# Kernel optimization log

Hardware: AMD Instinct MI355X
Metric: run time of the kernel (lower is better)

The kernel has to match this reference:

```python
import jax, jax.numpy as jnp
import numpy as np

B, Q, D, H, EF = 64, 300, 512, 8, 4
DH = D // H            # 64, per-head dim for scores
DV = (D * EF) // H     # 256, per-head value dim


def setup_inputs() -> dict:
    key = jax.random.key(0)
    ks = jax.random.split(key, 10)
    s = 0.02
    return {
        "query_feats": jax.random.normal(ks[0], (B, Q, D), jnp.float32),
        "bias": jax.random.normal(ks[1], (1, H, Q, Q), jnp.float32),
        "W_gen": jax.random.normal(ks[2], (D, D), jnp.float32) * s,
        "b_gen": jax.random.normal(ks[3], (D,), jnp.float32) * s,
        "W_val": jax.random.normal(ks[4], (D, D * EF), jnp.float32) * s,
        "b_val": jax.random.normal(ks[5], (D * EF,), jnp.float32) * s,
        "W_out": jax.random.normal(ks[6], (D * EF, D), jnp.float32) * s,
        "b_out": jax.random.normal(ks[7], (D,), jnp.float32) * s,
        "weight_bank": jnp.ones((1, H, Q, Q), jnp.float32) / np.sqrt(DH).astype(np.float32),
    }


def reference(query_feats, bias, W_gen, b_gen, W_val, b_val, W_out, b_out, weight_bank):
    bs, nq, d = query_feats.shape
    h = weight_bank.shape[1]
    # params_generator -> dynamic mixing matrix M: [bs, h, dh, nq]
    M = (query_feats @ W_gen + b_gen).reshape(bs, nq, h, -1).transpose(0, 2, 3, 1)
    # value: [bs, h, nq, dv]
    value = (query_feats @ W_val + b_val).reshape(bs, nq, h, -1).transpose(0, 2, 1, 3)
    # queries split per head: [bs, h, nq, dh]
    q = query_feats.reshape(bs, nq, h, -1).transpose(0, 2, 1, 3)
    # scores: [bs, h, nq, nq], scaled by learned weight bank + bias, GELU (exact), softmax
    scores = jnp.einsum('bhqd,bhdk->bhqk', q, M) * weight_bank + bias
    attn = jax.nn.softmax(jax.nn.gelu(scores, approximate=False), axis=-1)
    out = jnp.einsum('bhqk,bhkv->bhqv', attn, value)
    out = out.transpose(0, 2, 1, 3).reshape(bs, nq, -1)
    out = out @ W_out + b_out
    return out + query_feats
```

## Files before the change

### kernel.cpp

```cpp
#include <hip/hip_runtime.h>
#include <hip/hip_bf16.h>

typedef __attribute__((ext_vector_type(4))) float f32x4;
typedef __attribute__((ext_vector_type(8))) short s16x8;
typedef __attribute__((ext_vector_type(4))) short s16x4;
typedef __attribute__((ext_vector_type(4))) unsigned int u32x4;

#define MFMA16(A, B, C) __builtin_amdgcn_mfma_f32_16x16x32_bf16((A), (B), (C), 0, 0, 0)

#define GLDS16(gsrc, ldst) __builtin_amdgcn_global_load_lds(                   \
    (const __attribute__((address_space(1))) void*)(gsrc),                    \
    (__attribute__((address_space(3))) void*)(ldst), 16, 0, 0)

__device__ __forceinline__ ushort f2bf(float f) {
    __hip_bfloat16 h = __float2bfloat16(f);
    return *reinterpret_cast<ushort*>(&h);
}

__device__ __forceinline__ float exp_gelu(float x) {
    float u = x * x;
    float m = fmaf(-0.1029439065f, u, -2.3022154392f);
    float e2 = __builtin_amdgcn_exp2f(x * m);
    float g = x * __builtin_amdgcn_rcpf(1.0f + e2);
    return __expf(g);
}

__global__ __launch_bounds__(256) void k_prep(const float* __restrict__ qf,
                                              ushort* __restrict__ qf_bf,
                                              const float* __restrict__ W_gen,
                                              const float* __restrict__ W_val,
                                              const float* __restrict__ W_out,
                                              const float* __restrict__ wb,
                                              const float* __restrict__ bias,
                                              ushort* __restrict__ WgvT,
                                              ushort* __restrict__ WoT,
                                              unsigned int* __restrict__ wbbT,
                                              ushort* __restrict__ Vt) {
    __shared__ float tile[32][33];
    __shared__ float tb[32][33];
    int blk = blockIdx.x;
    int tx = threadIdx.x & 31, ty = threadIdx.x >> 5;
    if (blk < 9600) {
        int i = (blk * 256 + threadIdx.x) * 4;
        float4 v = *(const float4*)(qf + i);
        ushort4 o;
        o.x = f2bf(v.x); o.y = f2bf(v.y); o.z = f2bf(v.z); o.w = f2bf(v.w);
        *(ushort4*)(qf_bf + i) = o;
        return;
    }
    blk -= 9600;
    if (blk < 2304) {
        const float* w; ushort* wt; int K, N, kx, ny;
        if (blk < 256)       { w = W_gen; wt = WgvT;             K = 512;  N = 512;
                               kx = blk & 15;          ny = blk >> 4; }
        else if (blk < 1280) { w = W_val; wt = WgvT + 512 * 512; K = 512;  N = 2048;
                               int b2 = blk - 256;  kx = b2 & 15; ny = b2 >> 4; }
        else                 { w = W_out; wt = WoT;              K = 2048; N = 512;
                               int b2 = blk - 1280; kx = b2 & 63; ny = b2 >> 6; }
        int k0 = kx * 32, n0 = ny * 32;
        #pragma unroll
        for (int i = ty; i < 32; i += 8)
            tile[i][tx] = w[(size_t)(k0 + i) * N + n0 + tx];
        __syncthreads();
        #pragma unroll
        for (int i = ty; i < 32; i += 8)
            wt[(size_t)(n0 + i) * K + k0 + tx] = f2bf(tile[tx][i]);
        return;
    }
    blk -= 2304;
    if (blk < 800) {
        int h = blk / 100, rem = blk - h * 100;
        int kx = rem / 10, qx = rem - kx * 10;
        int k0 = kx * 32, q0 = qx * 32;
        #pragma unroll
        for (int i = ty; i < 32; i += 8)
            if (q0 + i < 300 && k0 + tx < 300) {
                size_t si = ((size_t)h * 300 + q0 + i) * 300 + k0 + tx;
                tile[i][tx] = wb[si];
                tb[i][tx]   = bias[si];
            }
        __syncthreads();
        #pragma unroll
        for (int i = ty; i < 32; i += 8)
            if (k0 + i < 300 && q0 + tx < 300) {
                int k = k0 + i;
                unsigned int pk = (unsigned int)f2bf(tile[tx][i])
                                | ((unsigned int)f2bf(tb[tx][i]) << 16);
                wbbT[(((size_t)h * 75 + (k >> 2)) * 300 + (q0 + tx)) * 4 + (k & 3)] = pk;
            }
        return;
    }
    blk -= 800;
    int tid = blk * 256 + threadIdx.x;
    int bh = tid >> 8, v = tid & 255;
    *(s16x4*)(Vt + (size_t)bh * 77824 + 73728 + v * 16 + 12) = (s16x4){0, 0, 0, 0};
}

template <int OUT>
__global__ __launch_bounds__(512, 2) void k_gemm256(const ushort* __restrict__ A,
                                                    const ushort* __restrict__ BT,
                                                    const float* __restrict__ b1,
                                                    const float* __restrict__ b2,
                                                    void* __restrict__ o1,
                                                    void* __restrict__ o2,
                                                    int K, int GY) {
    __shared__ __align__(16) ushort As[2][256 * 64];
    __shared__ __align__(16) ushort Bs[2][256 * 64];
    int id = blockIdx.x;
    int xcd = id & 7, s = id >> 3;
    int mxl = s / GY, ny = s - mxl * GY;
    int mx = xcd * 10 + mxl;
    if (mx >= 75) return;
    int m0 = mx * 256, n0g = ny * 256;

    int t = threadIdx.x, l = t & 63, w = t >> 6;
    int wr = w >> 2, wc = w & 3;
    int lr = l & 15, lg = l >> 4;

    int rsrc[4], ksrc[4];
    #pragma unroll
    for (int c8 = 0; c8 < 4; ++c8) {
        int o = (c8 * 512 + t) * 16;
        int op = o ^ (((o >> 7) & 7) << 4);
        rsrc[c8] = op >> 7;
        ksrc[c8] = (op & 127) >> 1;
    }

    auto stage = [&](int kt, int buf) {
        int k0 = kt * 64;
        ushort* AsB = &As[buf][0];
        ushort* BsB = &Bs[buf][0];
        #pragma unroll
        for (int c8 = 0; c8 < 4; ++c8) {
            int dst = (c8 * 512 + w * 64) * 8;
            GLDS16(A  + (size_t)(m0 + rsrc[c8]) * K + k0 + ksrc[c8], AsB + dst);
            GLDS16(BT + (size_t)(n0g + rsrc[c8]) * K + k0 + ksrc[c8], BsB + dst);
        }
    };

    f32x4 acc[8][4];
    #pragma unroll
    for (int i = 0; i < 8; ++i)
        #pragma unroll
        for (int j = 0; j < 4; ++j)
            acc[i][j] = (f32x4){0.f, 0.f, 0.f, 0.f};

    int NT = K >> 6;
    stage(0, 0);
    stage(1, 1);

    for (int kt = 0; kt < NT; ++kt) {
        if (kt + 1 < NT) asm volatile("s_waitcnt vmcnt(8)" ::: "memory");
        else             asm volatile("s_waitcnt vmcnt(0)" ::: "memory");
        __builtin_amdgcn_s_barrier();

        int cur = kt & 1;
        const char* Ab = (const char*)&As[cur][0];
        const char* Bb = (const char*)&Bs[cur][0];
        #pragma unroll
        for (int ks = 0; ks < 2; ++ks) {
            int kb = (ks * 64 + lg * 16) ^ ((lr & 7) << 4);
            s16x8 af[8], bfv[4];
            #pragma unroll
            for (int rt = 0; rt < 8; ++rt)
                af[rt] = *(const s16x8*)(Ab + (wr * 128 + rt * 16 + lr) * 128 + kb);
            #pragma unroll
            for (int ct = 0; ct < 4; ++ct)
                bfv[ct] = *(const s16x8*)(Bb + (wc * 64 + ct * 16 + lr) * 128 + kb);
            #pragma unroll
            for (int rt = 0; rt < 8; ++rt)
                #pragma unroll
                for (int ct = 0; ct < 4; ++ct)
                    acc[rt][ct] = MFMA16(af[rt], bfv[ct], acc[rt][ct]);
        }

        __builtin_amdgcn_s_barrier();
        if (kt + 2 < NT) stage(kt + 2, cur);
    }

    if (OUT == 0) {
        if (n0g < 512) {
            ushort* G = (ushort*)o1;
            #pragma unroll
            for (int rt = 0; rt < 8; ++rt)
                #pragma unroll
                for (int ct = 0; ct < 4; ++ct) {
                    int col = n0g + wc * 64 + ct * 16 + lr;
                    float bv = b1[col];
                    #pragma unroll
                    for (int rr = 0; rr < 4; ++rr) {
                        int row = m0 + wr * 128 + rt * 16 + lg * 4 + rr;
                        G[(size_t)row * 512 + col] = f2bf(acc[rt][ct][rr] + bv);
                    }
                }
        } else {
            ushort* Vt = (ushort*)o2;
            #pragma unroll
            for (int rt = 0; rt < 8; ++rt) {
                int rl0 = m0 + wr * 128 + rt * 16 + lg * 4;
                int bb = rl0 / 300, key0 = rl0 - bb * 300;
                #pragma unroll
                for (int ct = 0; ct < 4; ++ct) {
                    int colv = n0g - 512 + wc * 64 + ct * 16 + lr;
                    float bv = b2[colv];
                    int hh = colv >> 8, v = colv & 255;
                    s16x4 pw;
                    #pragma unroll
                    for (int rr = 0; rr < 4; ++rr)
                        pw[rr] = (short)f2bf(acc[rt][ct][rr] + bv);
                    size_t bhb = (size_t)(bb * 8 + hh) * 77824;
                    size_t addr = (key0 < 288)
                        ? bhb + (size_t)(key0 >> 5) * 8192 + v * 32 + (key0 & 31)
                        : bhb + 73728 + v * 16 + (key0 - 288);
                    *(s16x4*)(Vt + addr) = pw;
                }
            }
        }
    } else {
        float* out = (float*)o1;
        #pragma unroll
        for (int rt = 0; rt < 8; ++rt)
            #pragma unroll
            for (int ct = 0; ct < 4; ++ct) {
                int col = n0g + wc * 64 + ct * 16 + lr;
                float bv = b1[col];
                #pragma unroll
                for (int rr = 0; rr < 4; ++rr) {
                    int row = m0 + wr * 128 + rt * 16 + lg * 4 + rr;
                    size_t idx = (size_t)row * 512 + col;
                    out[idx] = acc[rt][ct][rr] + bv + b2[idx];
                }
            }
    }
}

__global__ __launch_bounds__(512, 6) void k_attn(const ushort* __restrict__ qf_bf,
                                                 const ushort* __restrict__ G_bf,
                                                 const ushort* __restrict__ Vt,
                                                 const unsigned int* __restrict__ wbb,
                                                 ushort* __restrict__ O) {
    __shared__ __align__(16) ushort P[64 * 320];
    __shared__ float partial[2][64];
    int id = blockIdx.x;
    int xcd = id & 7, s = id >> 3;
    int h = s / 40; int r2 = s - h * 40;
    int bi = r2 / 5, qt = r2 - bi * 5;
    int b = xcd * 8 + bi;

    int t = threadIdx.x, l = t & 63, w = t >> 6;
    int lr = l & 15, lg = l >> 4;
    int wq = w & 3, wk = w >> 2;

    auto p_addr = [&](int q, int k) -> ushort* {
        int byte = (q * 640 + k * 2) ^ ((q & 15) << 4);
        return (ushort*)((char*)P + byte);
    };

    int qr = min(qt * 64 + wq * 16 + lr, 299);
    const ushort* qp = qf_bf + ((size_t)(b * 300 + qr)) * 512 + h * 64 + lg * 8;
    s16x8 q0 = *(const s16x8*)(qp);
    s16x8 q1 = *(const s16x8*)(qp + 32);

    const unsigned int* wbbq = wbb + (size_t)h * 90000 + qr * 4;

    int qq = wq * 16 + lr;
    float ssum = 0.f;
    int ktlo = wk * 10, kthi = min(ktlo + 10, 18);
    const unsigned int* wp = wbbq + (size_t)(ktlo * 4 + lg) * 1200;
    const ushort* gp = G_bf + ((size_t)(b * 300) + ktlo * 16 + lr) * 512 + h * 64 + lg * 8;

    s16x8 g0 = *(const s16x8*)(gp);
    s16x8 g1 = *(const s16x8*)(gp + 32);
    u32x4 uv = *(const u32x4*)(wp);

    for (int kt = ktlo; kt < kthi - 1; ++kt) {
        const ushort* gpn = gp + 16 * 512;
        const unsigned int* wpn = wp + 4800;
        s16x8 ng0 = *(const s16x8*)(gpn);
        s16x8 ng1 = *(const s16x8*)(gpn + 32);
        u32x4 nuv = *(const u32x4*)(wpn);

        f32x4 a = (f32x4){0.f, 0.f, 0.f, 0.f};
        a = MFMA16(g0, q0, a);
        a = MFMA16(g1, q1, a);
        int kbase = kt * 16 + lg * 4;
        s16x4 pw;
        #pragma unroll
        for (int r = 0; r < 4; ++r) {
            unsigned int u = uv[r];
            float wv = __builtin_bit_cast(float, u << 16);
            float bv = __builtin_bit_cast(float, u & 0xffff0000u);
            float x = fmaf(a[r], wv, bv);
            float p = exp_gelu(x);
            ssum += p;
            pw[r] = (short)f2bf(p);
        }
        *(s16x4*)p_addr(qq, kbase) = pw;
        g0 = ng0; g1 = ng1; uv = nuv; gp = gpn; wp = wpn;
    }
    {
        f32x4 a = (f32x4){0.f, 0.f, 0.f, 0.f};
        a = MFMA16(g0, q0, a);
        a = MFMA16(g1, q1, a);
        int kbase = (kthi - 1) * 16 + lg * 4;
        s16x4 pw;
        #pragma unroll
        for (int r = 0; r < 4; ++r) {
            unsigned int u = uv[r];
            float wv = __builtin_bit_cast(float, u << 16);
            float bv = __builtin_bit_cast(float, u & 0xffff0000u);
            float x = fmaf(a[r], wv, bv);
            float p = exp_gelu(x);
            ssum += p;
            pw[r] = (short)f2bf(p);
        }
        *(s16x4*)p_addr(qq, kbase) = pw;
    }
    if (wk == 1) {
        int kcl = min(288 + lr, 299);
        const ushort* gpe = G_bf + ((size_t)(b * 300 + kcl)) * 512 + h * 64 + lg * 8;
        s16x8 e0 = *(const s16x8*)(gpe);
        s16x8 e1 = *(const s16x8*)(gpe + 32);
        f32x4 a = (f32x4){0.f, 0.f, 0.f, 0.f};
        a = MFMA16(e0, q0, a);
        a = MFMA16(e1, q1, a);
        int kbase = 288 + lg * 4;
        int g4 = min(72 + lg, 74);
        u32x4 ev = *(const u32x4*)(wbbq + (size_t)g4 * 1200);
        s16x4 pw;
        #pragma unroll
        for (int r = 0; r < 4; ++r) {
            unsigned int u = ev[r];
            float wv = __builtin_bit_cast(float, u << 16);
            float bv = __builtin_bit_cast(float, u & 0xffff0000u);
            float x = fmaf(a[r], wv, bv);
            float p = (lg < 3) ? exp_gelu(x) : 0.f;
            ssum += p;
            pw[r] = (short)f2bf(p);
        }
        *(s16x4*)p_addr(qq, kbase) = pw;
    }

    size_t bhb = (size_t)(b * 8 + h) * 77824;
    const ushort* vbase = Vt + bhb + (size_t)(w * 32) * 32 + lg * 8;
    s16x8 vb0 = *(const s16x8*)(vbase + lr * 32);
    s16x8 vb1 = *(const s16x8*)(vbase + (16 + lr) * 32);

    ssum += __shfl_xor(ssum, 16);
    ssum += __shfl_xor(ssum, 32);
    if (lg == 0) partial[wk][qq] = ssum;

    __syncthreads();

    f32x4 acc[4][2];
    #pragma unroll
    for (int qg = 0; qg < 4; ++qg)
        #pragma unroll
        for (int nt = 0; nt < 2; ++nt)
            acc[qg][nt] = (f32x4){0.f, 0.f, 0.f, 0.f};

    #pragma unroll
    for (int kc = 0; kc < 9; ++kc) {
        s16x8 nvb0, nvb1;
        if (kc < 8) {
            nvb0 = *(const s16x8*)(vbase + (size_t)(kc + 1) * 8192 + lr * 32);
            nvb1 = *(const s16x8*)(vbase + (size_t)(kc + 1) * 8192 + (16 + lr) * 32);
        }
        __builtin_amdgcn_s_setprio(1);
        #pragma unroll
        for (int qg = 0; qg < 4; ++qg) {
            s16x8 pa = *(const s16x8*)p_addr(qg * 16 + lr, kc * 32 + lg * 8);
            acc[qg][0] = MFMA16(pa, vb0, acc[qg][0]);
            acc[qg][1] = MFMA16(pa, vb1, acc[qg][1]);
        }
        __builtin_amdgcn_s_setprio(0);
        if (kc < 8) { vb0 = nvb0; vb1 = nvb1; }
    }
    {
        const ushort* c9 = Vt + bhb + 73728 + (size_t)(w * 32) * 16 + lg * 8;
        s16x8 cb0, cb1;
        if (lg < 2) {
            cb0 = *(const s16x8*)(c9 + lr * 16);
            cb1 = *(const s16x8*)(c9 + (16 + lr) * 16);
        } else {
            cb0 = (s16x8){0,0,0,0,0,0,0,0};
            cb1 = (s16x8){0,0,0,0,0,0,0,0};
        }
        #pragma unroll
        for (int qg = 0; qg < 4; ++qg) {
            s16x8 pa = (lg < 2)
                ? *(const s16x8*)p_addr(qg * 16 + lr, 288 + lg * 8)
                : (s16x8){0,0,0,0,0,0,0,0};
            acc[qg][0] = MFMA16(pa, cb0, acc[qg][0]);
            acc[qg][1] = MFMA16(pa, cb1, acc[qg][1]);
        }
    }

    #pragma unroll
    for (int qg = 0; qg < 4; ++qg)
        #pragma unroll
        for (int r = 0; r < 4; ++r) {
            int qloc = qg * 16 + lg * 4 + r;
            int q = qt * 64 + qloc;
            if (q < 300) {
                float iv = 1.0f / (partial[0][qloc] + partial[1][qloc]);
                #pragma unroll
                for (int nt = 0; nt < 2; ++nt) {
                    int v = w * 32 + nt * 16 + lr;
                    O[((size_t)(b * 300 + q)) * 2048 + h * 256 + v] =
                        f2bf(acc[qg][nt][r] * iv);
                }
            }
        }
}

extern "C" void kernel_launch(void* const* d_in, const int* in_sizes, int n_in,
                              void* d_out, int out_size, void* d_ws, size_t ws_size,
                              hipStream_t stream) {
    const float* qf    = (const float*)d_in[0];
    const float* bias  = (const float*)d_in[1];
    const float* W_gen = (const float*)d_in[2];
    const float* b_gen = (const float*)d_in[3];
    const float* W_val = (const float*)d_in[4];
    const float* b_val = (const float*)d_in[5];
    const float* W_out = (const float*)d_in[6];
    const float* b_out = (const float*)d_in[7];
    const float* wb    = (const float*)d_in[8];
    float* out = (float*)d_out;

    char* ws = (char*)d_ws;
    ushort* qf_bf = (ushort*)(ws);
    ushort* G_bf  = (ushort*)(ws + 19660800);
    ushort* Vt    = (ushort*)(ws + 39321600);
    ushort* O_bf  = (ushort*)(ws + 119013376);
    ushort* WgvT  = (ushort*)(ws + 197656576);
    ushort* WoT   = (ushort*)(ws + 200278016);
    unsigned int* wbbT = (unsigned int*)(ws + 202375168);

    k_prep<<<dim3(13216), dim3(256), 0, stream>>>(qf, qf_bf, W_gen, W_val, W_out,
                                                  wb, bias, WgvT, WoT, wbbT, Vt);

    k_gemm256<0><<<dim3(800), dim3(512), 0, stream>>>(qf_bf, WgvT, b_gen, b_val,
                                                      G_bf, Vt, 512, 10);

    k_attn<<<dim3(2560), dim3(512), 0, stream>>>(qf_bf, G_bf, Vt, wbbT, O_bf);

    k_gemm256<2><<<dim3(160), dim3(512), 0, stream>>>(O_bf, WoT, b_out, qf,
                                                      out, nullptr, 2048, 2);
}
```

Before: 266.1 us.

## Restructure GEMM k-loop into 4-stage half-tile pipeline with interleaved loads

Splits each 64-wide K tile of the 256x256 GEMM into two 32-wide halves held in a 4-deep LDS ring buffer, keeping three halves in flight. The global-to-LDS loads for the next stage are issued between the two MFMA groups, and the MFMA bursts run at raised wave priority via s_setprio. The aim is to hide load latency better and remove one barrier per tile. It uses a new XOR swizzle for 64-byte rows, which risks bank conflicts, and it relies on hand-counted vmcnt waits that must match the number of loads in flight.

```diff
diff --git a/kernel.cpp b/kernel.cpp
--- a/kernel.cpp
+++ b/kernel.cpp
@@ -104,8 +104,8 @@
                                                     void* __restrict__ o1,
                                                     void* __restrict__ o2,
                                                     int K, int GY) {
-    __shared__ __align__(16) ushort As[2][256 * 64];
-    __shared__ __align__(16) ushort Bs[2][256 * 64];
+    __shared__ __align__(16) ushort As4[4][256 * 32];
+    __shared__ __align__(16) ushort Bs4[4][256 * 32];
     int id = blockIdx.x;
     int xcd = id & 7, s = id >> 3;
     int mxl = s / GY, ny = s - mxl * GY;
@@ -117,25 +117,16 @@
     int wr = w >> 2, wc = w & 3;
     int lr = l & 15, lg = l >> 4;
 
-    int rsrc[4], ksrc[4];
-    #pragma unroll
-    for (int c8 = 0; c8 < 4; ++c8) {
-        int o = (c8 * 512 + t) * 16;
-        int op = o ^ (((o >> 7) & 7) << 4);
-        rsrc[c8] = op >> 7;
-        ksrc[c8] = (op & 127) >> 1;
-    }
-
-    auto stage = [&](int kt, int buf) {
-        int k0 = kt * 64;
-        ushort* AsB = &As[buf][0];
-        ushort* BsB = &Bs[buf][0];
-        #pragma unroll
-        for (int c8 = 0; c8 < 4; ++c8) {
-            int dst = (c8 * 512 + w * 64) * 8;
-            GLDS16(A  + (size_t)(m0 + rsrc[c8]) * K + k0 + ksrc[c8], AsB + dst);
-            GLDS16(BT + (size_t)(n0g + rsrc[c8]) * K + k0 + ksrc[c8], BsB + dst);
-        }
+    int drow = w * 16 + (l >> 2);
+    int kslog = (l & 3) ^ ((l >> 3) & 3);
+
+    auto stageH = [&](int H, int c) {
+        int buf = H & 3;
+        int kb = (H >> 1) * 64 + (H & 1) * 32 + kslog * 8;
+        int row = c * 128 + drow;
+        int dst = c * 4096 + w * 512;
+        GLDS16(A  + (size_t)(m0 + row) * K + kb, &As4[buf][dst]);
+        GLDS16(BT + (size_t)(n0g + row) * K + kb, &Bs4[buf][dst]);
     };
 
     f32x4 acc[8][4];
@@ -145,37 +136,59 @@
         for (int j = 0; j < 4; ++j)
             acc[i][j] = (f32x4){0.f, 0.f, 0.f, 0.f};
 
-    int NT = K >> 6;
-    stage(0, 0);
-    stage(1, 1);
-
-    for (int kt = 0; kt < NT; ++kt) {
-        if (kt + 1 < NT) asm volatile("s_waitcnt vmcnt(8)" ::: "memory");
-        else             asm volatile("s_waitcnt vmcnt(0)" ::: "memory");
-        __builtin_amdgcn_s_barrier();
-
-        int cur = kt & 1;
-        const char* Ab = (const char*)&As[cur][0];
-        const char* Bb = (const char*)&Bs[cur][0];
+    int NT = K >> 6, NH = NT * 2;
+    stageH(0, 0); stageH(0, 1);
+    stageH(1, 0); stageH(1, 1);
+    stageH(2, 0); stageH(2, 1);
+
+    int rsw = (lr >> 1) & 3;
+    for (int tt = 0; tt < NT; ++tt) {
         #pragma unroll
         for (int ks = 0; ks < 2; ++ks) {
-            int kb = (ks * 64 + lg * 16) ^ ((lr & 7) << 4);
-            s16x8 af[8], bfv[4];
-            #pragma unroll
-            for (int rt = 0; rt < 8; ++rt)
-                af[rt] = *(const s16x8*)(Ab + (wr * 128 + rt * 16 + lr) * 128 + kb);
-            #pragma unroll
-            for (int ct = 0; ct < 4; ++ct)
-                bfv[ct] = *(const s16x8*)(Bb + (wc * 64 + ct * 16 + lr) * 128 + kb);
-            #pragma unroll
-            for (int rt = 0; rt < 8; ++rt)
-                #pragma unroll
-                for (int ct = 0; ct < 4; ++ct)
-                    acc[rt][ct] = MFMA16(af[rt], bfv[ct], acc[rt][ct]);
-        }
-
-        __builtin_amdgcn_s_barrier();
-        if (kt + 2 < NT) stage(kt + 2, cur);
+            int H = 2 * tt + ks;
+            if (H + 2 < NH)      asm volatile("s_waitcnt vmcnt(8)" ::: "memory");
+            else if (H + 1 < NH) asm volatile("s_waitcnt vmcnt(4)" ::: "memory");
+            else                 asm volatile("s_waitcnt vmcnt(0)" ::: "memory");
+            __builtin_amdgcn_s_barrier();
+            int buf = H & 3;
+            const ushort* Ab = &As4[buf][0];
+            const ushort* Bb = &Bs4[buf][0];
+            bool more = (H + 3 < NH);
+
+            if (more) stageH(H + 3, 0);
+            s16x8 bfv[4], af[4];
+            #pragma unroll
+            for (int j = 0; j < 4; ++j) {
+                int row = wc * 64 + j * 16 + lr;
+                bfv[j] = *(const s16x8*)(Bb + row * 32 + ((lg ^ rsw) * 8));
+            }
+            #pragma unroll
+            for (int i = 0; i < 4; ++i) {
+                int row = wr * 128 + i * 16 + lr;
+                af[i] = *(const s16x8*)(Ab + row * 32 + ((lg ^ rsw) * 8));
+            }
+            __builtin_amdgcn_s_setprio(1);
+            #pragma unroll
+            for (int i = 0; i < 4; ++i)
+                #pragma unroll
+                for (int j = 0; j < 4; ++j)
+                    acc[i][j] = MFMA16(af[i], bfv[j], acc[i][j]);
+            __builtin_amdgcn_s_setprio(0);
+
+            if (more) stageH(H + 3, 1);
+            #pragma unroll
+            for (int i = 0; i < 4; ++i) {
+                int row = wr * 128 + (4 + i) * 16 + lr;
+                af[i] = *(const s16x8*)(Ab + row * 32 + ((lg ^ rsw) * 8));
+            }
+            __builtin_amdgcn_s_setprio(1);
+            #pragma unroll
+            for (int i = 0; i < 4; ++i)
+                #pragma unroll
+                for (int j = 0; j < 4; ++j)
+                    acc[4 + i][j] = MFMA16(af[i], bfv[j], acc[4 + i][j]);
+            __builtin_amdgcn_s_setprio(0);
+        }
     }
 
     if (OUT == 0) {
```

Result: slower. 290.7 us (+9.2%).
